# Performance work log

Measured on AMD Instinct MI355X. Metric: run time of the kernel, lower is better.

The kernel has to match this reference:

```python
import jax, jax.numpy as jnp
import numpy as np

B, T, F, U = 64, 2048, 256, 32


def setup_inputs() -> dict:
    key = jax.random.key(0)
    k0, k1, k2, k3, k4 = jax.random.split(key, 5)
    return {
        "x": jax.random.normal(k0, (B, T, F), jnp.float32),
        "kernel": jax.random.normal(k1, (F, U), jnp.float32) * (1.0 / np.sqrt(F)),
        "bias": jnp.zeros((U,), jnp.float32),
        "chain_kernel": jax.random.normal(k2, (U, U), jnp.float32) * 0.1,
        "left_boundary": jax.random.normal(k3, (U,), jnp.float32) * 0.1,
        "right_boundary": jax.random.normal(k4, (U,), jnp.float32) * 0.1,
    }


def _potentials(x, kernel, bias, left_boundary, right_boundary):
    # Dense (linear activation) + boundary energies at first/last timestep (mask=None path)
    pot = jnp.einsum("btf,fu->btu", x, kernel) + bias
    pot = pot.at[:, 0, :].add(left_boundary)
    pot = pot.at[:, -1, :].add(right_boundary)
    return pot  # [B, T, U]


def _viterbi(pot, chain):
    # pot: [B,T,U], chain: [U,U]; max-plus forward recursion + backtrack
    init = pot[:, 0]  # [B,U]

    def fwd(state, pot_t):
        # scores[b,i,j] = state[b,i] + chain[i,j]
        scores = state[:, :, None] + chain[None]
        bp = jnp.argmax(scores, axis=1).astype(jnp.int32)  # [B,U] backpointers
        new_state = jnp.max(scores, axis=1) + pot_t        # [B,U]
        return new_state, bp

    last, bps = jax.lax.scan(fwd, init, jnp.swapaxes(pot, 0, 1)[1:])  # bps: [T-1,B,U]
    best_score = jnp.max(last, axis=-1)                   # [B]
    last_tag = jnp.argmax(last, axis=-1).astype(jnp.int32)  # [B]

    def back(tag, bp_t):
        prev = jnp.take_along_axis(bp_t, tag[:, None], axis=1)[:, 0]
        return prev, prev

    _, tags_rev = jax.lax.scan(back, last_tag, bps[::-1])  # [T-1,B]
    tags = jnp.concatenate([tags_rev[::-1], last_tag[None]], axis=0)  # [T,B]
    return jnp.swapaxes(tags, 0, 1).astype(jnp.int32), best_score


def reference(x, kernel, bias, chain_kernel, left_boundary, right_boundary):
    pot = _potentials(x, kernel, bias, left_boundary, right_boundary)
    decoded, _ = _viterbi(pot, chain_kernel)
    return decoded  # [B, T] int32
```

## Files before the change

kernel.cpp:

```cpp
#include <hip/hip_runtime.h>
#include <hip/hip_bf16.h>
#include <cstdint>

#define BB 64
#define TT 2048
#define FD 256
#define UU 32

__global__ __launch_bounds__(256) void potentials_kernel(
    const float* __restrict__ x, const float* __restrict__ K,
    const float* __restrict__ bias, const float* __restrict__ lb,
    const float* __restrict__ rb, float* __restrict__ pot)
{
    __shared__ float Ks[FD * UU];
    __shared__ float xs[16 * FD];

    const int tid = threadIdx.x;
    for (int i = tid; i < FD * UU; i += 256) Ks[i] = K[i];

    const int u = tid & 31;
    const int g = tid >> 5;
    const float bu = bias[u];
    const float lu = lb[u];
    const float ru = rb[u];

    const int tiles = (BB * TT) / 16;
    for (int tile = blockIdx.x; tile < tiles; tile += gridDim.x) {
        const int row0 = tile * 16;
        __syncthreads();
        {
            const float4* src = (const float4*)(x + (size_t)row0 * FD);
            float4* dst = (float4*)xs;
            #pragma unroll
            for (int i = 0; i < 4; ++i) dst[tid + i * 256] = src[tid + i * 256];
        }
        __syncthreads();

        float acc0 = 0.f, acc1 = 0.f;
        #pragma unroll
        for (int f = 0; f < FD; f += 4) {
            const float4 xa = *(const float4*)&xs[g * FD + f];
            const float4 xb = *(const float4*)&xs[(g + 8) * FD + f];
            const float k0 = Ks[(f + 0) * UU + u];
            const float k1 = Ks[(f + 1) * UU + u];
            const float k2 = Ks[(f + 2) * UU + u];
            const float k3 = Ks[(f + 3) * UU + u];
            acc0 += xa.x * k0; acc0 += xa.y * k1; acc0 += xa.z * k2; acc0 += xa.w * k3;
            acc1 += xb.x * k0; acc1 += xb.y * k1; acc1 += xb.z * k2; acc1 += xb.w * k3;
        }

        const int ra = row0 + g;
        const int rbw = row0 + g + 8;
        const int ta = ra & (TT - 1);
        const int tb = rbw & (TT - 1);
        float adda = bu + (ta == 0 ? lu : 0.f) + (ta == TT - 1 ? ru : 0.f);
        float addb = bu + (tb == 0 ? lu : 0.f) + (tb == TT - 1 ? ru : 0.f);
        pot[(size_t)ra * UU + u]  = acc0 + adda;
        pot[(size_t)rbw * UU + u] = acc1 + addb;
    }
}

__global__ __launch_bounds__(64) void vit_values_kernel(
    const float* __restrict__ pot, const float* __restrict__ chain,
    float* __restrict__ chk)
{
    __shared__ __align__(16) float mbuf[64];

    const int lane = threadIdx.x;
    const int u = lane & 31;
    const int h = lane >> 5;
    const int b = blockIdx.x * 2 + h;
    const float* pb = pot + (size_t)b * TT * UU;
    const int h32 = h * 32;

    float cc[32];
    #pragma unroll
    for (int v = 0; v < 32; ++v) cc[v] = chain[v * UU + u];

    float s[32];
    #pragma unroll
    for (int v = 0; v < 32; ++v) s[v] = pb[v];

    auto step = [&](float potv, int t) {
        float a[32];
        #pragma unroll
        for (int v = 0; v < 32; ++v) a[v] = s[v] + cc[v];
        float m16[16];
        #pragma unroll
        for (int i = 0; i < 16; ++i) m16[i] = fmaxf(a[2*i], a[2*i+1]);
        float m8[8];
        #pragma unroll
        for (int i = 0; i < 8; ++i) m8[i] = fmaxf(m16[2*i], m16[2*i+1]);
        float m4[4];
        #pragma unroll
        for (int i = 0; i < 4; ++i) m4[i] = fmaxf(m8[2*i], m8[2*i+1]);
        const float pm = fmaxf(fmaxf(m4[0], m4[1]), fmaxf(m4[2], m4[3]));
        const float mm = pm + potv;

        mbuf[h32 + u] = mm;

        if ((t & 63) == 63) {
            const int wck = (t >> 6) + 1;
            chk[((size_t)b * 33 + wck) * UU + u] = mm;
        }

        const float4 x0 = *(const float4*)&mbuf[h32 + 0];
        const float4 x1 = *(const float4*)&mbuf[h32 + 4];
        const float4 x2 = *(const float4*)&mbuf[h32 + 8];
        const float4 x3 = *(const float4*)&mbuf[h32 + 12];
        const float4 x4 = *(const float4*)&mbuf[h32 + 16];
        const float4 x5 = *(const float4*)&mbuf[h32 + 20];
        const float4 x6 = *(const float4*)&mbuf[h32 + 24];
        const float4 x7 = *(const float4*)&mbuf[h32 + 28];
        s[0]=x0.x;  s[1]=x0.y;  s[2]=x0.z;  s[3]=x0.w;
        s[4]=x1.x;  s[5]=x1.y;  s[6]=x1.z;  s[7]=x1.w;
        s[8]=x2.x;  s[9]=x2.y;  s[10]=x2.z; s[11]=x2.w;
        s[12]=x3.x; s[13]=x3.y; s[14]=x3.z; s[15]=x3.w;
        s[16]=x4.x; s[17]=x4.y; s[18]=x4.z; s[19]=x4.w;
        s[20]=x5.x; s[21]=x5.y; s[22]=x5.z; s[23]=x5.w;
        s[24]=x6.x; s[25]=x6.y; s[26]=x6.z; s[27]=x6.w;
        s[28]=x7.x; s[29]=x7.y; s[30]=x7.z; s[31]=x7.w;
    };

    float pr[8], pn[8];
    #pragma unroll
    for (int j = 0; j < 8; ++j) pr[j] = pb[(1 + j) * UU + u];

    #pragma unroll 1
    for (int g = 0; g < 255; ++g) {
        #pragma unroll
        for (int j = 0; j < 8; ++j) {
            int tp = 9 + 8 * g + j;
            if (tp > TT - 1) tp = TT - 1;
            pn[j] = pb[tp * UU + u];
        }
        const int t0 = 1 + 8 * g;
        #pragma unroll
        for (int j = 0; j < 8; ++j)
            step(pr[j], t0 + j);
        #pragma unroll
        for (int j = 0; j < 8; ++j) pr[j] = pn[j];
    }
    #pragma unroll
    for (int j = 0; j < 7; ++j)
        step(pr[j], 2041 + j);
}

__global__ __launch_bounds__(64) void vit_window_kernel(
    const float* __restrict__ pot, const float* __restrict__ chain,
    const float* __restrict__ chk, unsigned char* __restrict__ Mg,
    unsigned char* __restrict__ bpg)
{
    __shared__ float potL[64 * 32];
    __shared__ float mbuf[32];

    const int lane = threadIdx.x;
    const int u = lane & 31;
    const int h = lane >> 5;
    const int hbase = 16 * h;
    const int w = blockIdx.x;
    const int b = blockIdx.y;
    const float* pb = pot + (size_t)b * TT * UU;
    const int r0 = 64 * w;

    {
        const float4* src = (const float4*)(pb + (size_t)r0 * UU);
        float4* dst = (float4*)potL;
        #pragma unroll
        for (int k = 0; k < 8; ++k) dst[lane + 64 * k] = src[lane + 64 * k];
    }
    __syncthreads();

    float cc[16];
    #pragma unroll
    for (int i = 0; i < 16; ++i) cc[i] = chain[(hbase + i) * UU + u];

    float s[16];
    if (w == 0) {
        #pragma unroll
        for (int i = 0; i < 16; ++i) s[i] = potL[hbase + i];
    } else {
        #pragma unroll
        for (int i = 0; i < 16; ++i) s[i] = chk[((size_t)b * 33 + w) * UU + hbase + i];
    }

    int orig = u;
    unsigned char* bb = bpg + (size_t)b * (TT - 1) * UU;

    const int tl0 = (w == 0) ? 1 : 0;
    #pragma unroll 1
    for (int tl = tl0; tl < 64; ++tl) {
        const int t = r0 + tl;
        const float potv = potL[tl * UU + u];

        float a[16];
        #pragma unroll
        for (int i = 0; i < 16; ++i) a[i] = s[i] + cc[i];

        float v8[8]; int i8[8];
        #pragma unroll
        for (int i = 0; i < 8; ++i) {
            const bool c = a[2*i+1] > a[2*i];
            v8[i] = c ? a[2*i+1] : a[2*i];
            i8[i] = c ? (2*i+1) : (2*i);
        }
        float v4[4]; int i4[4];
        #pragma unroll
        for (int i = 0; i < 4; ++i) {
            const bool c = v8[2*i+1] > v8[2*i];
            v4[i] = c ? v8[2*i+1] : v8[2*i];
            i4[i] = c ? i8[2*i+1] : i8[2*i];
        }
        float v2[2]; int i2[2];
        #pragma unroll
        for (int i = 0; i < 2; ++i) {
            const bool c = v4[2*i+1] > v4[2*i];
            v2[i] = c ? v4[2*i+1] : v4[2*i];
            i2[i] = c ? i4[2*i+1] : i4[2*i];
        }
        const bool cf = v2[1] > v2[0];
        const float pv = cf ? v2[1] : v2[0];
        const int pidx = hbase + (cf ? i2[1] : i2[0]);

        const float opv = __shfl_xor(pv, 32, 64);
        const int   opi = __shfl_xor(pidx, 32, 64);
        const bool take = h ? (opv >= pv) : (opv > pv);
        const int  mv   = take ? opi : pidx;
        const float mm  = fmaxf(pv, opv) + potv;

        if (h == 0) bb[(size_t)(t - 1) * UU + u] = (unsigned char)mv;
        orig = __shfl(orig, mv, 64);

        mbuf[u] = mm;
        const float4 x0 = *(const float4*)&mbuf[hbase + 0];
        const float4 x1 = *(const float4*)&mbuf[hbase + 4];
        const float4 x2 = *(const float4*)&mbuf[hbase + 8];
        const float4 x3 = *(const float4*)&mbuf[hbase + 12];
        s[0]=x0.x; s[1]=x0.y; s[2]=x0.z;  s[3]=x0.w;
        s[4]=x1.x; s[5]=x1.y; s[6]=x1.z;  s[7]=x1.w;
        s[8]=x2.x; s[9]=x2.y; s[10]=x2.z; s[11]=x2.w;
        s[12]=x3.x; s[13]=x3.y; s[14]=x3.z; s[15]=x3.w;
    }

    if (h == 0) Mg[(size_t)b * 1024 + w * UU + u] = (unsigned char)orig;
}

__global__ __launch_bounds__(64) void vit_backtrack_kernel(
    const float* __restrict__ chk, const unsigned char* __restrict__ Mg,
    const unsigned char* __restrict__ bpg, int* __restrict__ out)
{
    __shared__ unsigned char Ml[1024];
    __shared__ int tagw[32];

    const int lane = threadIdx.x;
    const int b = blockIdx.x;

    ((int4*)Ml)[lane] = ((const int4*)(Mg + (size_t)b * 1024))[lane];

    float fv = (lane < 32) ? chk[((size_t)b * 33 + 32) * UU + lane] : -INFINITY;
    int fi = lane & 31;
    #pragma unroll
    for (int mask = 16; mask >= 1; mask >>= 1) {
        const float ov = __shfl_xor(fv, mask, 64);
        const int oi = __shfl_xor(fi, mask, 64);
        if (ov > fv || (ov == fv && oi < fi)) { fv = ov; fi = oi; }
    }
    int bt = __shfl(fi, 0, 64);

    __syncthreads();
    #pragma unroll 1
    for (int w = 31; w >= 0; --w) {
        if (lane == 0) tagw[w] = bt;
        bt = Ml[w * 32 + bt];
    }
    __syncthreads();

    if (lane < 32) {
        const int w = lane;
        int tag = tagw[w];
        int t = w * 64 + 63;
        int* ob = out + (size_t)b * TT;
        const unsigned char* bb = bpg + (size_t)b * (TT - 1) * UU;
        ob[t] = tag;
        #pragma unroll 1
        for (; t >= w * 64 + 1; --t) {
            tag = bb[(size_t)(t - 1) * UU + tag];
            ob[t - 1] = tag;
        }
    }
}

extern "C" void kernel_launch(void* const* d_in, const int* in_sizes, int n_in,
                              void* d_out, int out_size, void* d_ws, size_t ws_size,
                              hipStream_t stream)
{
    const float* x     = (const float*)d_in[0];
    const float* K     = (const float*)d_in[1];
    const float* bias  = (const float*)d_in[2];
    const float* chain = (const float*)d_in[3];
    const float* lb    = (const float*)d_in[4];
    const float* rb    = (const float*)d_in[5];
    int* out = (int*)d_out;

    float* pot = (float*)d_ws;
    float* chk = pot + (size_t)BB * TT * UU;
    unsigned char* Mg  = (unsigned char*)(chk + (size_t)BB * 33 * UU);
    unsigned char* bpg = Mg + (size_t)BB * 32 * UU;

    potentials_kernel<<<1024, 256, 0, stream>>>(x, K, bias, lb, rb, pot);
    vit_values_kernel<<<BB / 2, 64, 0, stream>>>(pot, chain, chk);
    vit_window_kernel<<<dim3(32, BB), 64, 0, stream>>>(pot, chain, chk, Mg, bpg);
    vit_backtrack_kernel<<<BB, 64, 0, stream>>>(chk, Mg, bpg, out);
}
```

Baseline: 578.8 us.

## Split Viterbi max over lane pairs and stream x directly in potentials GEMV

The serial forward-values kernel now gives each batch its own block and splits each state's 32-way max across two lanes, combining the halves with a DPP quad swap. This halves the per-step dependent chain length and doubles the number of active blocks on the latency-bound recursion. The potentials kernel drops x staging in shared memory, reads x rows directly from global memory, and keeps a transposed, padded copy of K in LDS. It computes four rows per thread and sets an occupancy launch bound. The risk is more uncoalesced global traffic on x and extra register pressure.

New measurement: 562.3 us. -2.9%, faster.

```diff
diff --git a/kernel.cpp b/kernel.cpp
--- a/kernel.cpp
+++ b/kernel.cpp
@@ -7,119 +7,120 @@
 #define FD 256
 #define UU 32
 
-__global__ __launch_bounds__(256) void potentials_kernel(
+__global__ __launch_bounds__(256, 4) void potentials_kernel(
     const float* __restrict__ x, const float* __restrict__ K,
     const float* __restrict__ bias, const float* __restrict__ lb,
     const float* __restrict__ rb, float* __restrict__ pot)
 {
-    __shared__ float Ks[FD * UU];
-    __shared__ float xs[16 * FD];
+    __shared__ float Kt[UU * 260];
 
     const int tid = threadIdx.x;
-    for (int i = tid; i < FD * UU; i += 256) Ks[i] = K[i];
-
     const int u = tid & 31;
     const int g = tid >> 5;
+
+    for (int idx = tid; idx < FD * UU; idx += 256) {
+        const int f = idx >> 5;
+        const int uu = idx & 31;
+        Kt[uu * 260 + f] = K[idx];
+    }
+    __syncthreads();
+
     const float bu = bias[u];
     const float lu = lb[u];
     const float ru = rb[u];
 
-    const int tiles = (BB * TT) / 16;
+    const int tiles = (BB * TT) / 32;
     for (int tile = blockIdx.x; tile < tiles; tile += gridDim.x) {
-        const int row0 = tile * 16;
-        __syncthreads();
-        {
-            const float4* src = (const float4*)(x + (size_t)row0 * FD);
-            float4* dst = (float4*)xs;
-            #pragma unroll
-            for (int i = 0; i < 4; ++i) dst[tid + i * 256] = src[tid + i * 256];
-        }
-        __syncthreads();
-
-        float acc0 = 0.f, acc1 = 0.f;
-        #pragma unroll
+        const int row0 = tile * 32;
+        const float* x0 = x + (size_t)(row0 + g) * FD;
+
+        float acc0 = 0.f, acc1 = 0.f, acc2 = 0.f, acc3 = 0.f;
+        #pragma unroll 4
         for (int f = 0; f < FD; f += 4) {
-            const float4 xa = *(const float4*)&xs[g * FD + f];
-            const float4 xb = *(const float4*)&xs[(g + 8) * FD + f];
-            const float k0 = Ks[(f + 0) * UU + u];
-            const float k1 = Ks[(f + 1) * UU + u];
-            const float k2 = Ks[(f + 2) * UU + u];
-            const float k3 = Ks[(f + 3) * UU + u];
-            acc0 += xa.x * k0; acc0 += xa.y * k1; acc0 += xa.z * k2; acc0 += xa.w * k3;
-            acc1 += xb.x * k0; acc1 += xb.y * k1; acc1 += xb.z * k2; acc1 += xb.w * k3;
-        }
-
-        const int ra = row0 + g;
-        const int rbw = row0 + g + 8;
-        const int ta = ra & (TT - 1);
-        const int tb = rbw & (TT - 1);
-        float adda = bu + (ta == 0 ? lu : 0.f) + (ta == TT - 1 ? ru : 0.f);
-        float addb = bu + (tb == 0 ? lu : 0.f) + (tb == TT - 1 ? ru : 0.f);
-        pot[(size_t)ra * UU + u]  = acc0 + adda;
-        pot[(size_t)rbw * UU + u] = acc1 + addb;
-    }
+            const float4 kq = *(const float4*)&Kt[u * 260 + f];
+            const float4 xa = *(const float4*)(x0 + f);
+            const float4 xb = *(const float4*)(x0 + 8 * FD + f);
+            const float4 xc = *(const float4*)(x0 + 16 * FD + f);
+            const float4 xd = *(const float4*)(x0 + 24 * FD + f);
+            acc0 += xa.x * kq.x; acc0 += xa.y * kq.y; acc0 += xa.z * kq.z; acc0 += xa.w * kq.w;
+            acc1 += xb.x * kq.x; acc1 += xb.y * kq.y; acc1 += xb.z * kq.z; acc1 += xb.w * kq.w;
+            acc2 += xc.x * kq.x; acc2 += xc.y * kq.y; acc2 += xc.z * kq.z; acc2 += xc.w * kq.w;
+            acc3 += xd.x * kq.x; acc3 += xd.y * kq.y; acc3 += xd.z * kq.z; acc3 += xd.w * kq.w;
+        }
+
+        const int r0 = row0 + g;
+        const int r1 = r0 + 8;
+        const int r2 = r0 + 16;
+        const int r3 = r0 + 24;
+        const int t0 = r0 & (TT - 1), t1 = r1 & (TT - 1);
+        const int t2 = r2 & (TT - 1), t3 = r3 & (TT - 1);
+        pot[(size_t)r0 * UU + u] = acc0 + bu + (t0 == 0 ? lu : 0.f) + (t0 == TT - 1 ? ru : 0.f);
+        pot[(size_t)r1 * UU + u] = acc1 + bu + (t1 == 0 ? lu : 0.f) + (t1 == TT - 1 ? ru : 0.f);
+        pot[(size_t)r2 * UU + u] = acc2 + bu + (t2 == 0 ? lu : 0.f) + (t2 == TT - 1 ? ru : 0.f);
+        pot[(size_t)r3 * UU + u] = acc3 + bu + (t3 == 0 ? lu : 0.f) + (t3 == TT - 1 ? ru : 0.f);
+    }
+}
+
+__device__ __forceinline__ float quad_swap(float v) {
+    const int i = __float_as_int(v);
+    const int r = __builtin_amdgcn_update_dpp(i, i, 0xB1, 0xF, 0xF, true);
+    return __int_as_float(r);
 }
 
 __global__ __launch_bounds__(64) void vit_values_kernel(
     const float* __restrict__ pot, const float* __restrict__ chain,
     float* __restrict__ chk)
 {
-    __shared__ __align__(16) float mbuf[64];
+    __shared__ __align__(16) float mbuf[32];
 
     const int lane = threadIdx.x;
-    const int u = lane & 31;
-    const int h = lane >> 5;
-    const int b = blockIdx.x * 2 + h;
+    const int u = lane >> 1;
+    const int q = lane & 1;
+    const int qb = 16 * q;
+    const int b = blockIdx.x;
     const float* pb = pot + (size_t)b * TT * UU;
-    const int h32 = h * 32;
-
-    float cc[32];
-    #pragma unroll
-    for (int v = 0; v < 32; ++v) cc[v] = chain[v * UU + u];
-
-    float s[32];
-    #pragma unroll
-    for (int v = 0; v < 32; ++v) s[v] = pb[v];
+
+    float cc[16];
+    #pragma unroll
+    for (int i = 0; i < 16; ++i) cc[i] = chain[(qb + i) * UU + u];
+
+    float s[16];
+    {
+        const float4* s0 = (const float4*)(pb + qb);
+        #pragma unroll
+        for (int k = 0; k < 4; ++k) {
+            const float4 v = s0[k];
+            s[4*k+0] = v.x; s[4*k+1] = v.y; s[4*k+2] = v.z; s[4*k+3] = v.w;
+        }
+    }
 
     auto step = [&](float potv, int t) {
-        float a[32];
-        #pragma unroll
-        for (int v = 0; v < 32; ++v) a[v] = s[v] + cc[v];
-        float m16[16];
-        #pragma unroll
-        for (int i = 0; i < 16; ++i) m16[i] = fmaxf(a[2*i], a[2*i+1]);
+        float a[16];
+        #pragma unroll
+        for (int i = 0; i < 16; ++i) a[i] = s[i] + cc[i];
         float m8[8];
         #pragma unroll
-        for (int i = 0; i < 8; ++i) m8[i] = fmaxf(m16[2*i], m16[2*i+1]);
+        for (int i = 0; i < 8; ++i) m8[i] = fmaxf(a[2*i], a[2*i+1]);
         float m4[4];
         #pragma unroll
         for (int i = 0; i < 4; ++i) m4[i] = fmaxf(m8[2*i], m8[2*i+1]);
         const float pm = fmaxf(fmaxf(m4[0], m4[1]), fmaxf(m4[2], m4[3]));
-        const float mm = pm + potv;
-
-        mbuf[h32 + u] = mm;
-
-        if ((t & 63) == 63) {
-            const int wck = (t >> 6) + 1;
-            chk[((size_t)b * 33 + wck) * UU + u] = mm;
-        }
-
-        const float4 x0 = *(const float4*)&mbuf[h32 + 0];
-        const float4 x1 = *(const float4*)&mbuf[h32 + 4];
-        const float4 x2 = *(const float4*)&mbuf[h32 + 8];
-        const float4 x3 = *(const float4*)&mbuf[h32 + 12];
-        const float4 x4 = *(const float4*)&mbuf[h32 + 16];
-        const float4 x5 = *(const float4*)&mbuf[h32 + 20];
-        const float4 x6 = *(const float4*)&mbuf[h32 + 24];
-        const float4 x7 = *(const float4*)&mbuf[h32 + 28];
+        const float om = quad_swap(pm);
+        const float mm = fmaxf(pm, om) + potv;
+
+        mbuf[u] = mm;
+
+        if ((t & 63) == 63)
+            chk[((size_t)b * 33 + ((t >> 6) + 1)) * UU + u] = mm;
+
+        const float4 x0 = *(const float4*)&mbuf[qb + 0];
+        const float4 x1 = *(const float4*)&mbuf[qb + 4];
+        const float4 x2 = *(const float4*)&mbuf[qb + 8];
+        const float4 x3 = *(const float4*)&mbuf[qb + 12];
         s[0]=x0.x;  s[1]=x0.y;  s[2]=x0.z;  s[3]=x0.w;
         s[4]=x1.x;  s[5]=x1.y;  s[6]=x1.z;  s[7]=x1.w;
         s[8]=x2.x;  s[9]=x2.y;  s[10]=x2.z; s[11]=x2.w;
         s[12]=x3.x; s[13]=x3.y; s[14]=x3.z; s[15]=x3.w;
-        s[16]=x4.x; s[17]=x4.y; s[18]=x4.z; s[19]=x4.w;
-        s[20]=x5.x; s[21]=x5.y; s[22]=x5.z; s[23]=x5.w;
-        s[24]=x6.x; s[25]=x6.y; s[26]=x6.z; s[27]=x6.w;
-        s[28]=x7.x; s[29]=x7.y; s[30]=x7.z; s[31]=x7.w;
     };
 
     float pr[8], pn[8];
@@ -308,7 +309,7 @@
     unsigned char* bpg = Mg + (size_t)BB * 32 * UU;
 
     potentials_kernel<<<1024, 256, 0, stream>>>(x, K, bias, lb, rb, pot);
-    vit_values_kernel<<<BB / 2, 64, 0, stream>>>(pot, chain, chk);
+    vit_values_kernel<<<BB, 64, 0, stream>>>(pot, chain, chk);
     vit_window_kernel<<<dim3(32, BB), 64, 0, stream>>>(pot, chain, chk, Mg, bpg);
     vit_backtrack_kernel<<<BB, 64, 0, stream>>>(chk, Mg, bpg, out);
 }
```
